# Kernel tuning notes

Measured on AMD Instinct MI355X. Metric: run time of the kernel, lower is better.

The kernel has to match this reference:

```python
import jax, jax.numpy as jnp
import numpy as np

TTT_STEPS = 1
STABILITY_LAMBDA = 0.01
TTT_LR = 0.01

def setup_inputs() -> dict:
    key = jax.random.key(0)
    ks = jax.random.split(key, 4)
    B, T, H = 8, 4096, 1024
    D = H // 4
    scale1 = 1.0 / np.sqrt(H)
    scale2 = 1.0 / np.sqrt(D)
    return {
        "state": jax.random.normal(ks[0], (B, T, H), dtype=jnp.float32),
        "target": jax.random.normal(ks[1], (B, T, H), dtype=jnp.float32),
        "W1": jax.random.normal(ks[2], (H, D), dtype=jnp.float32) * scale1,
        "b1": jnp.zeros((D,), dtype=jnp.float32),
        "W2": jax.random.normal(ks[3], (D, H), dtype=jnp.float32) * scale2,
        "b2": jnp.zeros((H,), dtype=jnp.float32),
        "step_size": jnp.float32(TTT_LR),
    }

def reference(state, target, W1, b1, W2, b2, step_size):
    # TTT: one (or more) gradient-descent steps on the state, minimizing
    # per-token MSE of a 2-layer MLP reconstruction + stability penalty.
    orig_state = state  # detached anchor

    def loss_fn(s):
        h = jax.nn.relu(jnp.einsum("bth,hd->btd", s, W1) + b1)
        pred = jnp.einsum("btd,dh->bth", h, W2) + b2
        # F.mse_loss(..., 'none').mean(-1) then .mean() == global mean of sq err
        mse = jnp.mean((pred - target) ** 2)
        stab = STABILITY_LAMBDA * jnp.mean((s - orig_state) ** 2)
        return mse + stab

    for _ in range(TTT_STEPS):
        g = jax.grad(loss_fn)(state)
        state = state - step_size * g
    return state
```

## Files before the change

### kernel.cpp

```cpp
#include <hip/hip_runtime.h>
#include <hip/hip_bf16.h>


#define Hdim 1024
#define Ddim 256
#define NTOK 32768
#define MT   32

typedef __attribute__((ext_vector_type(8))) short bf16x8;
typedef __attribute__((ext_vector_type(4))) float f32x4;

static __device__ __forceinline__ unsigned short f2bf(float f) {
    unsigned u = __builtin_bit_cast(unsigned, f);
    u += 0x7FFFu + ((u >> 16) & 1u);
    return (unsigned short)(u >> 16);
}

__global__ void prep_weights(const float* __restrict__ W1, const float* __restrict__ W2,
                             unsigned short* __restrict__ w1, unsigned short* __restrict__ w1t,
                             unsigned short* __restrict__ w2, unsigned short* __restrict__ w2t) {
    int i = blockIdx.x * blockDim.x + threadIdx.x;
    if (i >= Hdim * Ddim) return;
    int h = i / Ddim, d = i - h * Ddim;
    unsigned short v1 = f2bf(W1[i]);
    w1[i] = v1;
    w1t[d * Hdim + h] = v1;
    unsigned short v2 = f2bf(W2[d * Hdim + h]);
    w2[d * Hdim + h] = v2;
    w2t[i] = v2;
}

__launch_bounds__(256, 2)
__global__ void ttt_fused(const float* __restrict__ state,
                          const float* __restrict__ target,
                          const float* __restrict__ b1,
                          const float* __restrict__ b2,
                          const float* __restrict__ step_size,
                          const unsigned short* __restrict__ w1,
                          const unsigned short* __restrict__ w1t,
                          const unsigned short* __restrict__ w2,
                          const unsigned short* __restrict__ w2t,
                          float* __restrict__ out) {
    __shared__ unsigned char eld[MT * Hdim * 2];
    __shared__ unsigned char hld[MT * Ddim * 2];

    const int tid  = threadIdx.x;
    const int lane = tid & 63;
    const int wv   = tid >> 6;
    const int lr16 = lane & 15;
    const int lhi  = lane >> 4;
    const int kof  = lhi * 8;
    const int m0   = blockIdx.x * MT;

    const f32x4 z4 = {0.f, 0.f, 0.f, 0.f};

    {
        f32x4 acc[2][4];
        #pragma unroll
        for (int mt = 0; mt < 2; ++mt)
            #pragma unroll
            for (int nt = 0; nt < 4; ++nt) acc[mt][nt] = z4;

        for (int kk = 0; kk < Hdim; kk += 32) {
            bf16x8 a[2];
            #pragma unroll
            for (int mt = 0; mt < 2; ++mt) {
                const float* sr = state + (size_t)(m0 + mt * 16 + lr16) * Hdim + kk + kof;
                float4 f0 = *(const float4*)sr;
                float4 f1 = *(const float4*)(sr + 4);
                bf16x8 av;
                av[0] = (short)f2bf(f0.x); av[1] = (short)f2bf(f0.y);
                av[2] = (short)f2bf(f0.z); av[3] = (short)f2bf(f0.w);
                av[4] = (short)f2bf(f1.x); av[5] = (short)f2bf(f1.y);
                av[6] = (short)f2bf(f1.z); av[7] = (short)f2bf(f1.w);
                a[mt] = av;
            }
            #pragma unroll
            for (int nt = 0; nt < 4; ++nt) {
                int col = wv * 64 + nt * 16 + lr16;
                bf16x8 b = *(const bf16x8*)(w1t + (size_t)col * Hdim + kk + kof);
                #pragma unroll
                for (int mt = 0; mt < 2; ++mt)
                    acc[mt][nt] = __builtin_amdgcn_mfma_f32_16x16x32_bf16(a[mt], b, acc[mt][nt], 0, 0, 0);
            }
        }
        float bias[4];
        #pragma unroll
        for (int nt = 0; nt < 4; ++nt) bias[nt] = b1[wv * 64 + nt * 16 + lr16];
        #pragma unroll
        for (int mt = 0; mt < 2; ++mt)
            #pragma unroll
            for (int nt = 0; nt < 4; ++nt) {
                int colg = wv * 64 + nt * 16 + lr16;
                #pragma unroll
                for (int i = 0; i < 4; ++i) {
                    int row = mt * 16 + lhi * 4 + i;
                    float hv = fmaxf(acc[mt][nt][i] + bias[nt], 0.f);
                    unsigned off = ((unsigned)(row * Ddim + colg) * 2u) ^ (unsigned)((row & 7) << 4);
                    *(unsigned short*)(hld + off) = f2bf(hv);
                }
            }
    }
    __syncthreads();

    {
        for (int nc = 0; nc < 4; ++nc) {
            const int cb = wv * 256 + nc * 64;
            f32x4 acc[2][4];
            #pragma unroll
            for (int mt = 0; mt < 2; ++mt)
                #pragma unroll
                for (int nt = 0; nt < 4; ++nt) acc[mt][nt] = z4;

            for (int kk = 0; kk < Ddim; kk += 32) {
                bf16x8 a[2];
                #pragma unroll
                for (int mt = 0; mt < 2; ++mt) {
                    int row = mt * 16 + lr16;
                    unsigned off = ((unsigned)(row * Ddim + kk + kof) * 2u) ^ (unsigned)((row & 7) << 4);
                    a[mt] = *(const bf16x8*)(hld + off);
                }
                #pragma unroll
                for (int nt = 0; nt < 4; ++nt) {
                    int col = cb + nt * 16 + lr16;
                    bf16x8 b = *(const bf16x8*)(w2t + (size_t)col * Ddim + kk + kof);
                    #pragma unroll
                    for (int mt = 0; mt < 2; ++mt)
                        acc[mt][nt] = __builtin_amdgcn_mfma_f32_16x16x32_bf16(a[mt], b, acc[mt][nt], 0, 0, 0);
                }
            }
            float bias[4];
            #pragma unroll
            for (int nt = 0; nt < 4; ++nt) bias[nt] = b2[cb + nt * 16 + lr16];
            #pragma unroll
            for (int nt = 0; nt < 4; ++nt) {
                int colg = cb + nt * 16 + lr16;
                #pragma unroll
                for (int mt = 0; mt < 2; ++mt)
                    #pragma unroll
                    for (int i = 0; i < 4; ++i) {
                        int row = mt * 16 + lhi * 4 + i;
                        float e = acc[mt][nt][i] + bias[nt]
                                - target[(size_t)(m0 + row) * Hdim + colg];
                        unsigned off = ((unsigned)(row * Hdim + colg) * 2u) ^ (unsigned)((row & 7) << 4);
                        *(unsigned short*)(eld + off) = f2bf(e);
                    }
            }
        }
    }
    __syncthreads();

    {
        f32x4 acc[2][4];
        #pragma unroll
        for (int mt = 0; mt < 2; ++mt)
            #pragma unroll
            for (int nt = 0; nt < 4; ++nt) acc[mt][nt] = z4;

        for (int kk = 0; kk < Hdim; kk += 32) {
            bf16x8 a[2];
            #pragma unroll
            for (int mt = 0; mt < 2; ++mt) {
                int row = mt * 16 + lr16;
                unsigned off = ((unsigned)(row * Hdim + kk + kof) * 2u) ^ (unsigned)((row & 7) << 4);
                a[mt] = *(const bf16x8*)(eld + off);
            }
            #pragma unroll
            for (int nt = 0; nt < 4; ++nt) {
                int col = wv * 64 + nt * 16 + lr16;
                bf16x8 b = *(const bf16x8*)(w2 + (size_t)col * Hdim + kk + kof);
                #pragma unroll
                for (int mt = 0; mt < 2; ++mt)
                    acc[mt][nt] = __builtin_amdgcn_mfma_f32_16x16x32_bf16(a[mt], b, acc[mt][nt], 0, 0, 0);
            }
        }
        #pragma unroll
        for (int mt = 0; mt < 2; ++mt)
            #pragma unroll
            for (int nt = 0; nt < 4; ++nt) {
                int colg = wv * 64 + nt * 16 + lr16;
                #pragma unroll
                for (int i = 0; i < 4; ++i) {
                    int row = mt * 16 + lhi * 4 + i;
                    unsigned off = ((unsigned)(row * Ddim + colg) * 2u) ^ (unsigned)((row & 7) << 4);
                    unsigned short hbits = *(const unsigned short*)(hld + off);
                    float dh = (hbits != 0) ? acc[mt][nt][i] : 0.f;
                    *(unsigned short*)(hld + off) = f2bf(dh);
                }
            }
    }
    __syncthreads();

    {
        const float cc = step_size[0] * (2.0f / (float)((long long)NTOK * Hdim));
        for (int nc = 0; nc < 4; ++nc) {
            const int cb = wv * 256 + nc * 64;
            f32x4 acc[2][4];
            #pragma unroll
            for (int mt = 0; mt < 2; ++mt)
                #pragma unroll
                for (int nt = 0; nt < 4; ++nt) acc[mt][nt] = z4;

            for (int kk = 0; kk < Ddim; kk += 32) {
                bf16x8 a[2];
                #pragma unroll
                for (int mt = 0; mt < 2; ++mt) {
                    int row = mt * 16 + lr16;
                    unsigned off = ((unsigned)(row * Ddim + kk + kof) * 2u) ^ (unsigned)((row & 7) << 4);
                    a[mt] = *(const bf16x8*)(hld + off);
                }
                #pragma unroll
                for (int nt = 0; nt < 4; ++nt) {
                    int col = cb + nt * 16 + lr16;
                    bf16x8 b = *(const bf16x8*)(w1 + (size_t)col * Ddim + kk + kof);
                    #pragma unroll
                    for (int mt = 0; mt < 2; ++mt)
                        acc[mt][nt] = __builtin_amdgcn_mfma_f32_16x16x32_bf16(a[mt], b, acc[mt][nt], 0, 0, 0);
                }
            }
            #pragma unroll
            for (int nt = 0; nt < 4; ++nt) {
                int colg = cb + nt * 16 + lr16;
                #pragma unroll
                for (int mt = 0; mt < 2; ++mt)
                    #pragma unroll
                    for (int i = 0; i < 4; ++i) {
                        int row = mt * 16 + lhi * 4 + i;
                        size_t gi = (size_t)(m0 + row) * Hdim + colg;
                        out[gi] = state[gi] - cc * acc[mt][nt][i];
                    }
            }
        }
    }
}

extern "C" void kernel_launch(void* const* d_in, const int* in_sizes, int n_in,
                              void* d_out, int out_size, void* d_ws, size_t ws_size,
                              hipStream_t stream) {
    const float* state     = (const float*)d_in[0];
    const float* target    = (const float*)d_in[1];
    const float* W1        = (const float*)d_in[2];
    const float* b1        = (const float*)d_in[3];
    const float* W2        = (const float*)d_in[4];
    const float* b2        = (const float*)d_in[5];
    const float* step_size = (const float*)d_in[6];
    float* out = (float*)d_out;

    unsigned short* w1  = (unsigned short*)d_ws;
    unsigned short* w1t = w1  + Hdim * Ddim;
    unsigned short* w2  = w1t + Hdim * Ddim;
    unsigned short* w2t = w2  + Hdim * Ddim;

    hipLaunchKernelGGL(prep_weights, dim3((Hdim * Ddim + 255) / 256), dim3(256), 0, stream,
                       W1, W2, w1, w1t, w2, w2t);
    hipLaunchKernelGGL(ttt_fused, dim3(NTOK / MT), dim3(256), 0, stream,
                       state, target, b1, b2, step_size, w1, w1t, w2, w2t, out);
}
```

Measured before the change: 656.2 us.

## Precompute W2·W2ᵀ Gram matrix to skip output-space GEMMs in backward pass

Rewrites the error backprop as h·G + c2 − target·W2ᵀ using a precomputed Gram matrix G = W2·W2ᵀ and c2 = W2·b2. This removes the forward decoder GEMM and its backward counterpart over the 1024-wide hidden, and the large error buffer in shared memory. The target projection is fused into the first K-loop alongside the encoder GEMM. Blocks now use 512 threads split into two row groups. The cost is bf16 rounding of G and target, which changes numerics.

```diff
diff --git a/kernel.cpp b/kernel.cpp
--- a/kernel.cpp
+++ b/kernel.cpp
@@ -17,218 +17,179 @@
 }
 
 __global__ void prep_weights(const float* __restrict__ W1, const float* __restrict__ W2,
-                             unsigned short* __restrict__ w1, unsigned short* __restrict__ w1t,
-                             unsigned short* __restrict__ w2, unsigned short* __restrict__ w2t) {
+                             unsigned short* __restrict__ w1t,
+                             unsigned short* __restrict__ w2b,
+                             unsigned short* __restrict__ w1b) {
     int i = blockIdx.x * blockDim.x + threadIdx.x;
     if (i >= Hdim * Ddim) return;
-    int h = i / Ddim, d = i - h * Ddim;
+    int h = i >> 8, d = i & 255;
     unsigned short v1 = f2bf(W1[i]);
-    w1[i] = v1;
+    w1b[i] = v1;
     w1t[d * Hdim + h] = v1;
-    unsigned short v2 = f2bf(W2[d * Hdim + h]);
-    w2[d * Hdim + h] = v2;
-    w2t[i] = v2;
-}
-
-__launch_bounds__(256, 2)
+    w2b[i] = f2bf(W2[i]);
+}
+
+__global__ void prep_G(const float* __restrict__ W2, const float* __restrict__ b2,
+                       unsigned short* __restrict__ Gb, float* __restrict__ c2) {
+    __shared__ float wd[Hdim];
+    __shared__ float red[4];
+    const int d = blockIdx.x;
+    const int t = threadIdx.x;
+    float4 v = *(const float4*)(W2 + (size_t)d * Hdim + t * 4);
+    *(float4*)(wd + t * 4) = v;
+    __syncthreads();
+    const float* wp = W2 + (size_t)t * Hdim;
+    float s = 0.f;
+    for (int h = 0; h < Hdim; h += 4) {
+        float4 a = *(const float4*)(wp + h);
+        s += a.x * wd[h] + a.y * wd[h + 1] + a.z * wd[h + 2] + a.w * wd[h + 3];
+    }
+    Gb[d * Ddim + t] = f2bf(s);
+    float4 bb = *(const float4*)(b2 + t * 4);
+    float p = bb.x * wd[t * 4] + bb.y * wd[t * 4 + 1] + bb.z * wd[t * 4 + 2] + bb.w * wd[t * 4 + 3];
+    #pragma unroll
+    for (int o = 32; o > 0; o >>= 1) p += __shfl_down(p, o);
+    if ((t & 63) == 0) red[t >> 6] = p;
+    __syncthreads();
+    if (t == 0) c2[d] = red[0] + red[1] + red[2] + red[3];
+}
+
+__launch_bounds__(512, 4)
 __global__ void ttt_fused(const float* __restrict__ state,
                           const float* __restrict__ target,
                           const float* __restrict__ b1,
-                          const float* __restrict__ b2,
                           const float* __restrict__ step_size,
-                          const unsigned short* __restrict__ w1,
                           const unsigned short* __restrict__ w1t,
-                          const unsigned short* __restrict__ w2,
-                          const unsigned short* __restrict__ w2t,
+                          const unsigned short* __restrict__ w2b,
+                          const unsigned short* __restrict__ w1b,
+                          const unsigned short* __restrict__ Gb,
+                          const float* __restrict__ c2,
                           float* __restrict__ out) {
-    __shared__ unsigned char eld[MT * Hdim * 2];
     __shared__ unsigned char hld[MT * Ddim * 2];
+    __shared__ unsigned char dld[MT * Ddim * 2];
 
     const int tid  = threadIdx.x;
     const int lane = tid & 63;
     const int wv   = tid >> 6;
+    const int mg   = wv >> 2;
+    const int w4   = wv & 3;
     const int lr16 = lane & 15;
     const int lhi  = lane >> 4;
     const int kof  = lhi * 8;
     const int m0   = blockIdx.x * MT;
+    const int rowA = mg * 16 + lr16;
 
     const f32x4 z4 = {0.f, 0.f, 0.f, 0.f};
 
-    {
-        f32x4 acc[2][4];
-        #pragma unroll
-        for (int mt = 0; mt < 2; ++mt)
-            #pragma unroll
-            for (int nt = 0; nt < 4; ++nt) acc[mt][nt] = z4;
-
-        for (int kk = 0; kk < Hdim; kk += 32) {
-            bf16x8 a[2];
-            #pragma unroll
-            for (int mt = 0; mt < 2; ++mt) {
-                const float* sr = state + (size_t)(m0 + mt * 16 + lr16) * Hdim + kk + kof;
-                float4 f0 = *(const float4*)sr;
-                float4 f1 = *(const float4*)(sr + 4);
-                bf16x8 av;
-                av[0] = (short)f2bf(f0.x); av[1] = (short)f2bf(f0.y);
-                av[2] = (short)f2bf(f0.z); av[3] = (short)f2bf(f0.w);
-                av[4] = (short)f2bf(f1.x); av[5] = (short)f2bf(f1.y);
-                av[6] = (short)f2bf(f1.z); av[7] = (short)f2bf(f1.w);
-                a[mt] = av;
-            }
+    f32x4 acc_h[4], acc_u[4];
+    #pragma unroll
+    for (int nt = 0; nt < 4; ++nt) { acc_h[nt] = z4; acc_u[nt] = z4; }
+
+    const float* sp0 = state  + (size_t)(m0 + rowA) * Hdim + kof;
+    const float* tp0 = target + (size_t)(m0 + rowA) * Hdim + kof;
+
+    for (int kk = 0; kk < Hdim; kk += 32) {
+        float4 s0 = *(const float4*)(sp0 + kk);
+        float4 s1 = *(const float4*)(sp0 + kk + 4);
+        float4 t0 = *(const float4*)(tp0 + kk);
+        float4 t1 = *(const float4*)(tp0 + kk + 4);
+        bf16x8 aS, aT;
+        aS[0] = (short)f2bf(s0.x); aS[1] = (short)f2bf(s0.y);
+        aS[2] = (short)f2bf(s0.z); aS[3] = (short)f2bf(s0.w);
+        aS[4] = (short)f2bf(s1.x); aS[5] = (short)f2bf(s1.y);
+        aS[6] = (short)f2bf(s1.z); aS[7] = (short)f2bf(s1.w);
+        aT[0] = (short)f2bf(t0.x); aT[1] = (short)f2bf(t0.y);
+        aT[2] = (short)f2bf(t0.z); aT[3] = (short)f2bf(t0.w);
+        aT[4] = (short)f2bf(t1.x); aT[5] = (short)f2bf(t1.y);
+        aT[6] = (short)f2bf(t1.z); aT[7] = (short)f2bf(t1.w);
+        #pragma unroll
+        for (int nt = 0; nt < 4; ++nt) {
+            int col = w4 * 64 + nt * 16 + lr16;
+            bf16x8 bw1 = *(const bf16x8*)(w1t + (size_t)col * Hdim + kk + kof);
+            acc_h[nt] = __builtin_amdgcn_mfma_f32_16x16x32_bf16(aS, bw1, acc_h[nt], 0, 0, 0);
+            bf16x8 bw2 = *(const bf16x8*)(w2b + (size_t)col * Hdim + kk + kof);
+            acc_u[nt] = __builtin_amdgcn_mfma_f32_16x16x32_bf16(aT, bw2, acc_u[nt], 0, 0, 0);
+        }
+    }
+
+    unsigned mask = 0;
+    #pragma unroll
+    for (int nt = 0; nt < 4; ++nt) {
+        int colg = w4 * 64 + nt * 16 + lr16;
+        float bias = b1[colg];
+        #pragma unroll
+        for (int i = 0; i < 4; ++i) {
+            int row = mg * 16 + lhi * 4 + i;
+            float z = acc_h[nt][i] + bias;
+            if (z > 0.f) mask |= 1u << (nt * 4 + i);
+            float hv = z > 0.f ? z : 0.f;
+            unsigned off = ((unsigned)(row * Ddim + colg) * 2u) ^ (unsigned)((row & 7) << 4);
+            *(unsigned short*)(hld + off) = f2bf(hv);
+        }
+    }
+    __syncthreads();
+
+    f32x4 acc_d[4];
+    #pragma unroll
+    for (int nt = 0; nt < 4; ++nt) {
+        int colg = w4 * 64 + nt * 16 + lr16;
+        float c2v = c2[colg];
+        #pragma unroll
+        for (int i = 0; i < 4; ++i) acc_d[nt][i] = c2v - acc_u[nt][i];
+    }
+    #pragma unroll
+    for (int kk = 0; kk < Ddim; kk += 32) {
+        unsigned offa = ((unsigned)(rowA * Ddim + kk + kof) * 2u) ^ (unsigned)((rowA & 7) << 4);
+        bf16x8 aH = *(const bf16x8*)(hld + offa);
+        #pragma unroll
+        for (int nt = 0; nt < 4; ++nt) {
+            int col = w4 * 64 + nt * 16 + lr16;
+            bf16x8 bG = *(const bf16x8*)(Gb + (size_t)col * Ddim + kk + kof);
+            acc_d[nt] = __builtin_amdgcn_mfma_f32_16x16x32_bf16(aH, bG, acc_d[nt], 0, 0, 0);
+        }
+    }
+    #pragma unroll
+    for (int nt = 0; nt < 4; ++nt) {
+        int colg = w4 * 64 + nt * 16 + lr16;
+        #pragma unroll
+        for (int i = 0; i < 4; ++i) {
+            int row = mg * 16 + lhi * 4 + i;
+            float dh = ((mask >> (nt * 4 + i)) & 1u) ? acc_d[nt][i] : 0.f;
+            unsigned off = ((unsigned)(row * Ddim + colg) * 2u) ^ (unsigned)((row & 7) << 4);
+            *(unsigned short*)(dld + off) = f2bf(dh);
+        }
+    }
+    __syncthreads();
+
+    const float cc = step_size[0] * (2.0f / (float)((long long)NTOK * Hdim));
+    bf16x8 aD[8];
+    #pragma unroll
+    for (int kq = 0; kq < 8; ++kq) {
+        unsigned off = ((unsigned)(rowA * Ddim + kq * 32 + kof) * 2u) ^ (unsigned)((rowA & 7) << 4);
+        aD[kq] = *(const bf16x8*)(dld + off);
+    }
+    for (int nc = 0; nc < 4; ++nc) {
+        const int cb = w4 * 256 + nc * 64;
+        f32x4 acc[4];
+        #pragma unroll
+        for (int nt = 0; nt < 4; ++nt) acc[nt] = z4;
+        #pragma unroll
+        for (int kq = 0; kq < 8; ++kq) {
             #pragma unroll
             for (int nt = 0; nt < 4; ++nt) {
-                int col = wv * 64 + nt * 16 + lr16;
-                bf16x8 b = *(const bf16x8*)(w1t + (size_t)col * Hdim + kk + kof);
-                #pragma unroll
-                for (int mt = 0; mt < 2; ++mt)
-                    acc[mt][nt] = __builtin_amdgcn_mfma_f32_16x16x32_bf16(a[mt], b, acc[mt][nt], 0, 0, 0);
+                int col = cb + nt * 16 + lr16;
+                bf16x8 bW = *(const bf16x8*)(w1b + (size_t)col * Ddim + kq * 32 + kof);
+                acc[nt] = __builtin_amdgcn_mfma_f32_16x16x32_bf16(aD[kq], bW, acc[nt], 0, 0, 0);
             }
         }
-        float bias[4];
-        #pragma unroll
-        for (int nt = 0; nt < 4; ++nt) bias[nt] = b1[wv * 64 + nt * 16 + lr16];
-        #pragma unroll
-        for (int mt = 0; mt < 2; ++mt)
+        #pragma unroll
+        for (int nt = 0; nt < 4; ++nt) {
+            int colg = cb + nt * 16 + lr16;
             #pragma unroll
-            for (int nt = 0; nt < 4; ++nt) {
-                int colg = wv * 64 + nt * 16 + lr16;
-                #pragma unroll
-                for (int i = 0; i < 4; ++i) {
-                    int row = mt * 16 + lhi * 4 + i;
-                    float hv = fmaxf(acc[mt][nt][i] + bias[nt], 0.f);
-                    unsigned off = ((unsigned)(row * Ddim + colg) * 2u) ^ (unsigned)((row & 7) << 4);
-                    *(unsigned short*)(hld + off) = f2bf(hv);
-                }
-            }
-    }
-    __syncthreads();
-
-    {
-        for (int nc = 0; nc < 4; ++nc) {
-            const int cb = wv * 256 + nc * 64;
-            f32x4 acc[2][4];
-            #pragma unroll
-            for (int mt = 0; mt < 2; ++mt)
-                #pragma unroll
-                for (int nt = 0; nt < 4; ++nt) acc[mt][nt] = z4;
-
-            for (int kk = 0; kk < Ddim; kk += 32) {
-                bf16x8 a[2];
-                #pragma unroll
-                for (int mt = 0; mt < 2; ++mt) {
-                    int row = mt * 16 + lr16;
-                    unsigned off = ((unsigned)(row * Ddim + kk + kof) * 2u) ^ (unsigned)((row & 7) << 4);
-                    a[mt] = *(const bf16x8*)(hld + off);
-                }
-                #pragma unroll
-                for (int nt = 0; nt < 4; ++nt) {
-                    int col = cb + nt * 16 + lr16;
-                    bf16x8 b = *(const bf16x8*)(w2t + (size_t)col * Ddim + kk + kof);
-                    #pragma unroll
-                    for (int mt = 0; mt < 2; ++mt)
-                        acc[mt][nt] = __builtin_amdgcn_mfma_f32_16x16x32_bf16(a[mt], b, acc[mt][nt], 0, 0, 0);
-                }
-            }
-            float bias[4];
-            #pragma unroll
-            for (int nt = 0; nt < 4; ++nt) bias[nt] = b2[cb + nt * 16 + lr16];
-            #pragma unroll
-            for (int nt = 0; nt < 4; ++nt) {
-                int colg = cb + nt * 16 + lr16;
-                #pragma unroll
-                for (int mt = 0; mt < 2; ++mt)
-                    #pragma unroll
-                    for (int i = 0; i < 4; ++i) {
-                        int row = mt * 16 + lhi * 4 + i;
-                        float e = acc[mt][nt][i] + bias[nt]
-                                - target[(size_t)(m0 + row) * Hdim + colg];
-                        unsigned off = ((unsigned)(row * Hdim + colg) * 2u) ^ (unsigned)((row & 7) << 4);
-                        *(unsigned short*)(eld + off) = f2bf(e);
-                    }
-            }
-        }
-    }
-    __syncthreads();
-
-    {
-        f32x4 acc[2][4];
-        #pragma unroll
-        for (int mt = 0; mt < 2; ++mt)
-            #pragma unroll
-            for (int nt = 0; nt < 4; ++nt) acc[mt][nt] = z4;
-
-        for (int kk = 0; kk < Hdim; kk += 32) {
-            bf16x8 a[2];
-            #pragma unroll
-            for (int mt = 0; mt < 2; ++mt) {
-                int row = mt * 16 + lr16;
-                unsigned off = ((unsigned)(row * Hdim + kk + kof) * 2u) ^ (unsigned)((row & 7) << 4);
-                a[mt] = *(const bf16x8*)(eld + off);
-            }
-            #pragma unroll
-            for (int nt = 0; nt < 4; ++nt) {
-                int col = wv * 64 + nt * 16 + lr16;
-                bf16x8 b = *(const bf16x8*)(w2 + (size_t)col * Hdim + kk + kof);
-                #pragma unroll
-                for (int mt = 0; mt < 2; ++mt)
-                    acc[mt][nt] = __builtin_amdgcn_mfma_f32_16x16x32_bf16(a[mt], b, acc[mt][nt], 0, 0, 0);
-            }
-        }
-        #pragma unroll
-        for (int mt = 0; mt < 2; ++mt)
-            #pragma unroll
-            for (int nt = 0; nt < 4; ++nt) {
-                int colg = wv * 64 + nt * 16 + lr16;
-                #pragma unroll
-                for (int i = 0; i < 4; ++i) {
-                    int row = mt * 16 + lhi * 4 + i;
-                    unsigned off = ((unsigned)(row * Ddim + colg) * 2u) ^ (unsigned)((row & 7) << 4);
-                    unsigned short hbits = *(const unsigned short*)(hld + off);
-                    float dh = (hbits != 0) ? acc[mt][nt][i] : 0.f;
-                    *(unsigned short*)(hld + off) = f2bf(dh);
-                }
-            }
-    }
-    __syncthreads();
-
-    {
-        const float cc = step_size[0] * (2.0f / (float)((long long)NTOK * Hdim));
-        for (int nc = 0; nc < 4; ++nc) {
-            const int cb = wv * 256 + nc * 64;
-            f32x4 acc[2][4];
-            #pragma unroll
-            for (int mt = 0; mt < 2; ++mt)
-                #pragma unroll
-                for (int nt = 0; nt < 4; ++nt) acc[mt][nt] = z4;
-
-            for (int kk = 0; kk < Ddim; kk += 32) {
-                bf16x8 a[2];
-                #pragma unroll
-                for (int mt = 0; mt < 2; ++mt) {
-                    int row = mt * 16 + lr16;
-                    unsigned off = ((unsigned)(row * Ddim + kk + kof) * 2u) ^ (unsigned)((row & 7) << 4);
-                    a[mt] = *(const bf16x8*)(hld + off);
-                }
-                #pragma unroll
-                for (int nt = 0; nt < 4; ++nt) {
-                    int col = cb + nt * 16 + lr16;
-                    bf16x8 b = *(const bf16x8*)(w1 + (size_t)col * Ddim + kk + kof);
-                    #pragma unroll
-                    for (int mt = 0; mt < 2; ++mt)
-                        acc[mt][nt] = __builtin_amdgcn_mfma_f32_16x16x32_bf16(a[mt], b, acc[mt][nt], 0, 0, 0);
-                }
-            }
-            #pragma unroll
-            for (int nt = 0; nt < 4; ++nt) {
-                int colg = cb + nt * 16 + lr16;
-                #pragma unroll
-                for (int mt = 0; mt < 2; ++mt)
-                    #pragma unroll
-                    for (int i = 0; i < 4; ++i) {
-                        int row = mt * 16 + lhi * 4 + i;
-                        size_t gi = (size_t)(m0 + row) * Hdim + colg;
-                        out[gi] = state[gi] - cc * acc[mt][nt][i];
-                    }
+            for (int i = 0; i < 4; ++i) {
+                int row = mg * 16 + lhi * 4 + i;
+                size_t gi = (size_t)(m0 + row) * Hdim + colg;
+                out[gi] = state[gi] - cc * acc[nt][i];
             }
         }
     }
@@ -246,13 +207,15 @@
     const float* step_size = (const float*)d_in[6];
     float* out = (float*)d_out;
 
-    unsigned short* w1  = (unsigned short*)d_ws;
-    unsigned short* w1t = w1  + Hdim * Ddim;
-    unsigned short* w2  = w1t + Hdim * Ddim;
-    unsigned short* w2t = w2  + Hdim * Ddim;
+    unsigned short* w1t = (unsigned short*)d_ws;
+    unsigned short* w2b = w1t + Hdim * Ddim;
+    unsigned short* w1b = w2b + Hdim * Ddim;
+    unsigned short* Gb  = w1b + Hdim * Ddim;
+    float*          c2  = (float*)(Gb + Ddim * Ddim);
 
     hipLaunchKernelGGL(prep_weights, dim3((Hdim * Ddim + 255) / 256), dim3(256), 0, stream,
-                       W1, W2, w1, w1t, w2, w2t);
-    hipLaunchKernelGGL(ttt_fused, dim3(NTOK / MT), dim3(256), 0, stream,
-                       state, target, b1, b2, step_size, w1, w1t, w2, w2t, out);
-}
+                       W1, W2, w1t, w2b, w1b);
+    hipLaunchKernelGGL(prep_G, dim3(Ddim), dim3(256), 0, stream, W2, b2, Gb, c2);
+    hipLaunchKernelGGL(ttt_fused, dim3(NTOK / MT), dim3(512), 0, stream,
+                       state, target, b1, step_size, w1t, w2b, w1b, Gb, c2, out);
+}
```

New measurement: 763.4 us. 16.3% more time.

## Fold W2 into Gram matrix and fuse state/target projections with LDS-staged tiles

Applied to the files above, without the earlier changes.

Rewrites the backward pass algebraically. W2·(W2ᵀh + b2 − target) becomes h·G + c2 − target·W2ᵀ, with G = W2W2ᵀ and c2 = W2·b2 precomputed, so the H-wide error tensor is never materialized. The state·W1 and target·W2ᵀ projections run in one K-loop over 128-token tiles with LDS double-buffered staging and 512 threads. This removes one large GEMM and the error round-trip through LDS. In exchange it adds prep kernels, uses more LDS per block, and rounds G to bf16, which shifts the numerical error.

```diff
diff --git a/kernel.cpp b/kernel.cpp
--- a/kernel.cpp
+++ b/kernel.cpp
@@ -5,10 +5,13 @@
 #define Hdim 1024
 #define Ddim 256
 #define NTOK 32768
-#define MT   32
+#define MT   128
+#define KC   64
 
 typedef __attribute__((ext_vector_type(8))) short bf16x8;
 typedef __attribute__((ext_vector_type(4))) float f32x4;
+typedef __attribute__((ext_vector_type(4))) unsigned int u32x4;
+typedef unsigned short ushort_t;
 
 static __device__ __forceinline__ unsigned short f2bf(float f) {
     unsigned u = __builtin_bit_cast(unsigned, f);
@@ -16,222 +19,320 @@
     return (unsigned short)(u >> 16);
 }
 
-__global__ void prep_weights(const float* __restrict__ W1, const float* __restrict__ W2,
-                             unsigned short* __restrict__ w1, unsigned short* __restrict__ w1t,
-                             unsigned short* __restrict__ w2, unsigned short* __restrict__ w2t) {
-    int i = blockIdx.x * blockDim.x + threadIdx.x;
+static __device__ __forceinline__ bf16x8 pack8(float4 a, float4 b) {
+    bf16x8 v;
+    v[0] = (short)f2bf(a.x); v[1] = (short)f2bf(a.y);
+    v[2] = (short)f2bf(a.z); v[3] = (short)f2bf(a.w);
+    v[4] = (short)f2bf(b.x); v[5] = (short)f2bf(b.y);
+    v[6] = (short)f2bf(b.z); v[7] = (short)f2bf(b.w);
+    return v;
+}
+
+static __device__ __forceinline__ unsigned swz(unsigned byte_off, int row) {
+    return byte_off ^ ((unsigned)(row & 7) << 4);
+}
+
+__global__ void prep_copy(const float* __restrict__ W1, const float* __restrict__ W2,
+                          ushort_t* __restrict__ w1b, ushort_t* __restrict__ w2b) {
+    int i = (blockIdx.x * 256 + threadIdx.x) * 8;
     if (i >= Hdim * Ddim) return;
-    int h = i / Ddim, d = i - h * Ddim;
-    unsigned short v1 = f2bf(W1[i]);
-    w1[i] = v1;
-    w1t[d * Hdim + h] = v1;
-    unsigned short v2 = f2bf(W2[d * Hdim + h]);
-    w2[d * Hdim + h] = v2;
-    w2t[i] = v2;
-}
-
-__launch_bounds__(256, 2)
+    float4 a0 = *(const float4*)(W1 + i), a1 = *(const float4*)(W1 + i + 4);
+    *(bf16x8*)(w1b + i) = pack8(a0, a1);
+    float4 c0 = *(const float4*)(W2 + i), c1 = *(const float4*)(W2 + i + 4);
+    *(bf16x8*)(w2b + i) = pack8(c0, c1);
+}
+
+__global__ void prep_t(const float* __restrict__ W1, ushort_t* __restrict__ w1t) {
+    __shared__ ushort_t tile[64][72];
+    const int h0 = blockIdx.x * 64, d0 = blockIdx.y * 64;
+    const int t = threadIdx.x;
+    const int r = t >> 2, c4 = (t & 3) * 16;
+    #pragma unroll
+    for (int j = 0; j < 4; ++j) {
+        float4 v = *(const float4*)(W1 + (size_t)(h0 + r) * Ddim + d0 + c4 + j * 4);
+        tile[r][c4 + j * 4 + 0] = f2bf(v.x);
+        tile[r][c4 + j * 4 + 1] = f2bf(v.y);
+        tile[r][c4 + j * 4 + 2] = f2bf(v.z);
+        tile[r][c4 + j * 4 + 3] = f2bf(v.w);
+    }
+    __syncthreads();
+    const int dr = t >> 2, hc = (t & 3) * 16;
+    bf16x8 o0, o1;
+    #pragma unroll
+    for (int j = 0; j < 8; ++j) o0[j] = (short)tile[hc + j][dr];
+    #pragma unroll
+    for (int j = 0; j < 8; ++j) o1[j] = (short)tile[hc + 8 + j][dr];
+    *(bf16x8*)(w1t + (size_t)(d0 + dr) * Hdim + h0 + hc)     = o0;
+    *(bf16x8*)(w1t + (size_t)(d0 + dr) * Hdim + h0 + hc + 8) = o1;
+}
+
+__launch_bounds__(512, 2)
+__global__ void prep_G(const ushort_t* __restrict__ w2b, const float* __restrict__ W2,
+                       const float* __restrict__ b2, ushort_t* __restrict__ Gb,
+                       float* __restrict__ c2) {
+    const int tid = threadIdx.x, lane = tid & 63, wv = tid >> 6;
+    const int lr16 = lane & 15, lhi = lane >> 4;
+    const int rbase = blockIdx.x * 128 + (wv >> 2) * 64;
+    const int ngb = (wv & 3) * 64;
+    const f32x4 z4 = {0.f, 0.f, 0.f, 0.f};
+    f32x4 acc[4][4];
+    #pragma unroll
+    for (int mt = 0; mt < 4; ++mt)
+        #pragma unroll
+        for (int nt = 0; nt < 4; ++nt) acc[mt][nt] = z4;
+    #pragma unroll 4
+    for (int kk = 0; kk < 32; ++kk) {
+        bf16x8 aA[4], bB[4];
+        #pragma unroll
+        for (int mt = 0; mt < 4; ++mt)
+            aA[mt] = *(const bf16x8*)(w2b + (size_t)(rbase + mt * 16 + lr16) * Hdim + kk * 32 + lhi * 8);
+        #pragma unroll
+        for (int nt = 0; nt < 4; ++nt)
+            bB[nt] = *(const bf16x8*)(w2b + (size_t)(ngb + nt * 16 + lr16) * Hdim + kk * 32 + lhi * 8);
+        #pragma unroll
+        for (int mt = 0; mt < 4; ++mt)
+            #pragma unroll
+            for (int nt = 0; nt < 4; ++nt)
+                acc[mt][nt] = __builtin_amdgcn_mfma_f32_16x16x32_bf16(aA[mt], bB[nt], acc[mt][nt], 0, 0, 0);
+    }
+    #pragma unroll
+    for (int mt = 0; mt < 4; ++mt)
+        #pragma unroll
+        for (int nt = 0; nt < 4; ++nt) {
+            int col = ngb + nt * 16 + lr16;
+            #pragma unroll
+            for (int i = 0; i < 4; ++i) {
+                int row = rbase + mt * 16 + lhi * 4 + i;
+                Gb[row * Ddim + col] = f2bf(acc[mt][nt][i]);
+            }
+        }
+    if (blockIdx.x == 0 && tid < 256) {
+        const float* wp = W2 + (size_t)tid * Hdim;
+        float s0 = 0.f, s1 = 0.f;
+        for (int h = 0; h < Hdim; h += 8) {
+            float4 a = *(const float4*)(wp + h), b = *(const float4*)(wp + h + 4);
+            float4 x = *(const float4*)(b2 + h), y = *(const float4*)(b2 + h + 4);
+            s0 += a.x * x.x + a.y * x.y + a.z * x.z + a.w * x.w;
+            s1 += b.x * y.x + b.y * y.y + b.z * y.z + b.w * y.w;
+        }
+        c2[tid] = s0 + s1;
+    }
+}
+
+__launch_bounds__(512, 2)
 __global__ void ttt_fused(const float* __restrict__ state,
                           const float* __restrict__ target,
-                          const float* __restrict__ b1,
-                          const float* __restrict__ b2,
+                          const float* __restrict__ b1g,
                           const float* __restrict__ step_size,
-                          const unsigned short* __restrict__ w1,
-                          const unsigned short* __restrict__ w1t,
-                          const unsigned short* __restrict__ w2,
-                          const unsigned short* __restrict__ w2t,
+                          const ushort_t* __restrict__ w1t,
+                          const ushort_t* __restrict__ w2b,
+                          const ushort_t* __restrict__ w1b,
+                          const ushort_t* __restrict__ Gb,
+                          const float* __restrict__ c2,
                           float* __restrict__ out) {
-    __shared__ unsigned char eld[MT * Hdim * 2];
-    __shared__ unsigned char hld[MT * Ddim * 2];
+    __shared__ __align__(16) char smem[131072];
+    char* const sS  = smem;
+    char* const sT  = smem + 16384;
+    char* const sW1 = smem + 32768;
+    char* const sW2 = smem + 65536;
+    char* const hls = smem;
+    char* const dls = smem + 65536;
 
     const int tid  = threadIdx.x;
     const int lane = tid & 63;
     const int wv   = tid >> 6;
+    const int mgb  = (wv >> 2) * 64;
+    const int ng   = wv & 3;
+    const int ngb  = ng * 64;
     const int lr16 = lane & 15;
     const int lhi  = lane >> 4;
-    const int kof  = lhi * 8;
     const int m0   = blockIdx.x * MT;
 
+    const int srow = tid >> 2;
+    const int sc4  = (tid & 3) * 16;
+    const int wrow = tid >> 1;
+    const int wce  = (tid & 1) * 32;
+    const float* const spS = state  + (size_t)(m0 + srow) * Hdim + sc4;
+    const float* const spT = target + (size_t)(m0 + srow) * Hdim + sc4;
+    const ushort_t* const wpA = w1t + (size_t)wrow * Hdim + wce;
+    const ushort_t* const wpB = w2b + (size_t)wrow * Hdim + wce;
+    const unsigned offS0 = swz((unsigned)(srow * 128 + sc4 * 2), srow);
+    const unsigned offS1 = swz((unsigned)(srow * 128 + sc4 * 2 + 16), srow);
+    unsigned offW[4];
+    #pragma unroll
+    for (int j = 0; j < 4; ++j) offW[j] = swz((unsigned)(wrow * 128 + wce * 2 + j * 16), wrow);
+
     const f32x4 z4 = {0.f, 0.f, 0.f, 0.f};
-
+    f32x4 acc_h[4][4], acc_u[4][4];
+    #pragma unroll
+    for (int mt = 0; mt < 4; ++mt)
+        #pragma unroll
+        for (int nt = 0; nt < 4; ++nt) { acc_h[mt][nt] = z4; acc_u[mt][nt] = z4; }
+
+    float4 ps[4], pt[4];
+
+#define ISSUE(kc) { \
+    _Pragma("unroll") for (int j = 0; j < 4; ++j) ps[j] = *(const float4*)(spS + (kc) * KC + j * 4); \
+    _Pragma("unroll") for (int j = 0; j < 4; ++j) pt[j] = *(const float4*)(spT + (kc) * KC + j * 4); }
+
+#define STAGE(kc) { \
+    u32x4 pw[8]; \
+    _Pragma("unroll") for (int j = 0; j < 4; ++j) pw[j]     = *(const u32x4*)(wpA + (kc) * KC + j * 8); \
+    _Pragma("unroll") for (int j = 0; j < 4; ++j) pw[4 + j] = *(const u32x4*)(wpB + (kc) * KC + j * 8); \
+    *(bf16x8*)(sS + offS0) = pack8(ps[0], ps[1]); \
+    *(bf16x8*)(sS + offS1) = pack8(ps[2], ps[3]); \
+    *(bf16x8*)(sT + offS0) = pack8(pt[0], pt[1]); \
+    *(bf16x8*)(sT + offS1) = pack8(pt[2], pt[3]); \
+    _Pragma("unroll") for (int j = 0; j < 4; ++j) *(u32x4*)(sW1 + offW[j]) = pw[j]; \
+    _Pragma("unroll") for (int j = 0; j < 4; ++j) *(u32x4*)(sW2 + offW[j]) = pw[4 + j]; }
+
+#define COMPUTE() { \
+    _Pragma("unroll") for (int kk = 0; kk < 2; ++kk) { \
+        bf16x8 aS[4], aT[4], b1v[4], b2v[4]; \
+        _Pragma("unroll") for (int mt = 0; mt < 4; ++mt) { \
+            int r = mgb + mt * 16 + lr16; \
+            unsigned off = swz((unsigned)(r * 128 + kk * 64 + lhi * 16), r); \
+            aS[mt] = *(const bf16x8*)(sS + off); \
+            aT[mt] = *(const bf16x8*)(sT + off); \
+        } \
+        _Pragma("unroll") for (int nt = 0; nt < 4; ++nt) { \
+            int c = ngb + nt * 16 + lr16; \
+            unsigned off = swz((unsigned)(c * 128 + kk * 64 + lhi * 16), c); \
+            b1v[nt] = *(const bf16x8*)(sW1 + off); \
+            b2v[nt] = *(const bf16x8*)(sW2 + off); \
+        } \
+        _Pragma("unroll") for (int mt = 0; mt < 4; ++mt) \
+            _Pragma("unroll") for (int nt = 0; nt < 4; ++nt) { \
+                acc_h[mt][nt] = __builtin_amdgcn_mfma_f32_16x16x32_bf16(aS[mt], b1v[nt], acc_h[mt][nt], 0, 0, 0); \
+                acc_u[mt][nt] = __builtin_amdgcn_mfma_f32_16x16x32_bf16(aT[mt], b2v[nt], acc_u[mt][nt], 0, 0, 0); \
+            } \
+    } }
+
+    ISSUE(0);
+    STAGE(0);
+    ISSUE(1);
+    __syncthreads();
+    for (int kc = 0; kc < Hdim / KC; ++kc) {
+        COMPUTE();
+        __syncthreads();
+        if (kc < Hdim / KC - 1) {
+            STAGE(kc + 1);
+            if (kc < Hdim / KC - 2) ISSUE(kc + 2);
+            __syncthreads();
+        }
+    }
+
+    unsigned long long mask = 0ULL;
     {
-        f32x4 acc[2][4];
-        #pragma unroll
-        for (int mt = 0; mt < 2; ++mt)
-            #pragma unroll
-            for (int nt = 0; nt < 4; ++nt) acc[mt][nt] = z4;
-
-        for (int kk = 0; kk < Hdim; kk += 32) {
-            bf16x8 a[2];
-            #pragma unroll
-            for (int mt = 0; mt < 2; ++mt) {
-                const float* sr = state + (size_t)(m0 + mt * 16 + lr16) * Hdim + kk + kof;
-                float4 f0 = *(const float4*)sr;
-                float4 f1 = *(const float4*)(sr + 4);
-                bf16x8 av;
-                av[0] = (short)f2bf(f0.x); av[1] = (short)f2bf(f0.y);
-                av[2] = (short)f2bf(f0.z); av[3] = (short)f2bf(f0.w);
-                av[4] = (short)f2bf(f1.x); av[5] = (short)f2bf(f1.y);
-                av[6] = (short)f2bf(f1.z); av[7] = (short)f2bf(f1.w);
-                a[mt] = av;
-            }
+        float bia[4];
+        #pragma unroll
+        for (int nt = 0; nt < 4; ++nt) bia[nt] = b1g[ngb + nt * 16 + lr16];
+        #pragma unroll
+        for (int mt = 0; mt < 4; ++mt)
             #pragma unroll
             for (int nt = 0; nt < 4; ++nt) {
-                int col = wv * 64 + nt * 16 + lr16;
-                bf16x8 b = *(const bf16x8*)(w1t + (size_t)col * Hdim + kk + kof);
-                #pragma unroll
-                for (int mt = 0; mt < 2; ++mt)
-                    acc[mt][nt] = __builtin_amdgcn_mfma_f32_16x16x32_bf16(a[mt], b, acc[mt][nt], 0, 0, 0);
-            }
-        }
-        float bias[4];
-        #pragma unroll
-        for (int nt = 0; nt < 4; ++nt) bias[nt] = b1[wv * 64 + nt * 16 + lr16];
-        #pragma unroll
-        for (int mt = 0; mt < 2; ++mt)
+                int col = ngb + nt * 16 + lr16;
+                #pragma unroll
+                for (int i = 0; i < 4; ++i) {
+                    int row = mgb + mt * 16 + lhi * 4 + i;
+                    float z = acc_h[mt][nt][i] + bia[nt];
+                    float hv = z > 0.f ? z : 0.f;
+                    if (z > 0.f) mask |= 1ULL << (mt * 16 + nt * 4 + i);
+                    *(ushort_t*)(hls + swz((unsigned)(row * 512 + col * 2), row)) = f2bf(hv);
+                }
+            }
+    }
+    __syncthreads();
+
+    {
+        f32x4 acc_d[4][4];
+        #pragma unroll
+        for (int nt = 0; nt < 4; ++nt) {
+            float cv = c2[ngb + nt * 16 + lr16];
+            #pragma unroll
+            for (int mt = 0; mt < 4; ++mt)
+                #pragma unroll
+                for (int i = 0; i < 4; ++i) acc_d[mt][nt][i] = cv - acc_u[mt][nt][i];
+        }
+        #pragma unroll
+        for (int kk = 0; kk < 8; ++kk) {
+            bf16x8 aH[4], bG[4];
+            #pragma unroll
+            for (int mt = 0; mt < 4; ++mt) {
+                int r = mgb + mt * 16 + lr16;
+                aH[mt] = *(const bf16x8*)(hls + swz((unsigned)(r * 512 + kk * 64 + lhi * 16), r));
+            }
             #pragma unroll
             for (int nt = 0; nt < 4; ++nt) {
-                int colg = wv * 64 + nt * 16 + lr16;
+                int c = ngb + nt * 16 + lr16;
+                bG[nt] = *(const bf16x8*)(Gb + (size_t)c * Ddim + kk * 32 + lhi * 8);
+            }
+            #pragma unroll
+            for (int mt = 0; mt < 4; ++mt)
+                #pragma unroll
+                for (int nt = 0; nt < 4; ++nt)
+                    acc_d[mt][nt] = __builtin_amdgcn_mfma_f32_16x16x32_bf16(aH[mt], bG[nt], acc_d[mt][nt], 0, 0, 0);
+        }
+        #pragma unroll
+        for (int mt = 0; mt < 4; ++mt)
+            #pragma unroll
+            for (int nt = 0; nt < 4; ++nt) {
+                int col = ngb + nt * 16 + lr16;
                 #pragma unroll
                 for (int i = 0; i < 4; ++i) {
-                    int row = mt * 16 + lhi * 4 + i;
-                    float hv = fmaxf(acc[mt][nt][i] + bias[nt], 0.f);
-                    unsigned off = ((unsigned)(row * Ddim + colg) * 2u) ^ (unsigned)((row & 7) << 4);
-                    *(unsigned short*)(hld + off) = f2bf(hv);
+                    int row = mgb + mt * 16 + lhi * 4 + i;
+                    float v = ((mask >> (mt * 16 + nt * 4 + i)) & 1ULL) ? acc_d[mt][nt][i] : 0.f;
+                    *(ushort_t*)(dls + swz((unsigned)(row * 512 + col * 2), row)) = f2bf(v);
                 }
             }
     }
     __syncthreads();
 
     {
+        const float cc = step_size[0] * (2.0f / ((float)NTOK * (float)Hdim));
         for (int nc = 0; nc < 4; ++nc) {
-            const int cb = wv * 256 + nc * 64;
-            f32x4 acc[2][4];
-            #pragma unroll
-            for (int mt = 0; mt < 2; ++mt)
+            const int cb = ng * 256 + nc * 64;
+            f32x4 acc[4][4];
+            #pragma unroll
+            for (int mt = 0; mt < 4; ++mt)
                 #pragma unroll
                 for (int nt = 0; nt < 4; ++nt) acc[mt][nt] = z4;
-
-            for (int kk = 0; kk < Ddim; kk += 32) {
-                bf16x8 a[2];
-                #pragma unroll
-                for (int mt = 0; mt < 2; ++mt) {
-                    int row = mt * 16 + lr16;
-                    unsigned off = ((unsigned)(row * Ddim + kk + kof) * 2u) ^ (unsigned)((row & 7) << 4);
-                    a[mt] = *(const bf16x8*)(hld + off);
+            #pragma unroll
+            for (int kq = 0; kq < 8; ++kq) {
+                bf16x8 aD[4], bW[4];
+                #pragma unroll
+                for (int mt = 0; mt < 4; ++mt) {
+                    int r = mgb + mt * 16 + lr16;
+                    aD[mt] = *(const bf16x8*)(dls + swz((unsigned)(r * 512 + kq * 64 + lhi * 16), r));
                 }
                 #pragma unroll
                 for (int nt = 0; nt < 4; ++nt) {
-                    int col = cb + nt * 16 + lr16;
-                    bf16x8 b = *(const bf16x8*)(w2t + (size_t)col * Ddim + kk + kof);
+                    int c = cb + nt * 16 + lr16;
+                    bW[nt] = *(const bf16x8*)(w1b + (size_t)c * Ddim + kq * 32 + lhi * 8);
+                }
+                #pragma unroll
+                for (int mt = 0; mt < 4; ++mt)
                     #pragma unroll
-                    for (int mt = 0; mt < 2; ++mt)
-                        acc[mt][nt] = __builtin_amdgcn_mfma_f32_16x16x32_bf16(a[mt], b, acc[mt][nt], 0, 0, 0);
-                }
-            }
-            float bias[4];
-            #pragma unroll
-            for (int nt = 0; nt < 4; ++nt) bias[nt] = b2[cb + nt * 16 + lr16];
+                    for (int nt = 0; nt < 4; ++nt)
+                        acc[mt][nt] = __builtin_amdgcn_mfma_f32_16x16x32_bf16(aD[mt], bW[nt], acc[mt][nt], 0, 0, 0);
+            }
             #pragma unroll
             for (int nt = 0; nt < 4; ++nt) {
-                int colg = cb + nt * 16 + lr16;
-                #pragma unroll
-                for (int mt = 0; mt < 2; ++mt)
+                int col = cb + nt * 16 + lr16;
+                #pragma unroll
+                for (int mt = 0; mt < 4; ++mt)
                     #pragma unroll
                     for (int i = 0; i < 4; ++i) {
-                        int row = mt * 16 + lhi * 4 + i;
-                        float e = acc[mt][nt][i] + bias[nt]
-                                - target[(size_t)(m0 + row) * Hdim + colg];
-                        unsigned off = ((unsigned)(row * Hdim + colg) * 2u) ^ (unsigned)((row & 7) << 4);
-                        *(unsigned short*)(eld + off) = f2bf(e);
-                    }
-            }
-        }
-    }
-    __syncthreads();
-
-    {
-        f32x4 acc[2][4];
-        #pragma unroll
-        for (int mt = 0; mt < 2; ++mt)
-            #pragma unroll
-            for (int nt = 0; nt < 4; ++nt) acc[mt][nt] = z4;
-
-        for (int kk = 0; kk < Hdim; kk += 32) {
-            bf16x8 a[2];
-            #pragma unroll
-            for (int mt = 0; mt < 2; ++mt) {
-                int row = mt * 16 + lr16;
-                unsigned off = ((unsigned)(row * Hdim + kk + kof) * 2u) ^ (unsigned)((row & 7) << 4);
-                a[mt] = *(const bf16x8*)(eld + off);
-            }
-            #pragma unroll
-            for (int nt = 0; nt < 4; ++nt) {
-                int col = wv * 64 + nt * 16 + lr16;
-                bf16x8 b = *(const bf16x8*)(w2 + (size_t)col * Hdim + kk + kof);
-                #pragma unroll
-                for (int mt = 0; mt < 2; ++mt)
-                    acc[mt][nt] = __builtin_amdgcn_mfma_f32_16x16x32_bf16(a[mt], b, acc[mt][nt], 0, 0, 0);
-            }
-        }
-        #pragma unroll
-        for (int mt = 0; mt < 2; ++mt)
-            #pragma unroll
-            for (int nt = 0; nt < 4; ++nt) {
-                int colg = wv * 64 + nt * 16 + lr16;
-                #pragma unroll
-                for (int i = 0; i < 4; ++i) {
-                    int row = mt * 16 + lhi * 4 + i;
-                    unsigned off = ((unsigned)(row * Ddim + colg) * 2u) ^ (unsigned)((row & 7) << 4);
-                    unsigned short hbits = *(const unsigned short*)(hld + off);
-                    float dh = (hbits != 0) ? acc[mt][nt][i] : 0.f;
-                    *(unsigned short*)(hld + off) = f2bf(dh);
-                }
-            }
-    }
-    __syncthreads();
-
-    {
-        const float cc = step_size[0] * (2.0f / (float)((long long)NTOK * Hdim));
-        for (int nc = 0; nc < 4; ++nc) {
-            const int cb = wv * 256 + nc * 64;
-            f32x4 acc[2][4];
-            #pragma unroll
-            for (int mt = 0; mt < 2; ++mt)
-                #pragma unroll
-                for (int nt = 0; nt < 4; ++nt) acc[mt][nt] = z4;
-
-            for (int kk = 0; kk < Ddim; kk += 32) {
-                bf16x8 a[2];
-                #pragma unroll
-                for (int mt = 0; mt < 2; ++mt) {
-                    int row = mt * 16 + lr16;
-                    unsigned off = ((unsigned)(row * Ddim + kk + kof) * 2u) ^ (unsigned)((row & 7) << 4);
-                    a[mt] = *(const bf16x8*)(hld + off);
-                }
-                #pragma unroll
-                for (int nt = 0; nt < 4; ++nt) {
-                    int col = cb + nt * 16 + lr16;
-                    bf16x8 b = *(const bf16x8*)(w1 + (size_t)col * Ddim + kk + kof);
-                    #pragma unroll
-                    for (int mt = 0; mt < 2; ++mt)
-                        acc[mt][nt] = __builtin_amdgcn_mfma_f32_16x16x32_bf16(a[mt], b, acc[mt][nt], 0, 0, 0);
-                }
-            }
-            #pragma unroll
-            for (int nt = 0; nt < 4; ++nt) {
-                int colg = cb + nt * 16 + lr16;
-                #pragma unroll
-                for (int mt = 0; mt < 2; ++mt)
-                    #pragma unroll
-                    for (int i = 0; i < 4; ++i) {
-                        int row = mt * 16 + lhi * 4 + i;
-                        size_t gi = (size_t)(m0 + row) * Hdim + colg;
+                        int row = mgb + mt * 16 + lhi * 4 + i;
+                        size_t gi = (size_t)(m0 + row) * Hdim + col;
                         out[gi] = state[gi] - cc * acc[mt][nt][i];
                     }
             }
         }
     }
+#undef ISSUE
+#undef STAGE
+#undef COMPUTE
 }
 
 extern "C" void kernel_launch(void* const* d_in, const int* in_sizes, int n_in,
@@ -246,13 +347,15 @@
     const float* step_size = (const float*)d_in[6];
     float* out = (float*)d_out;
 
-    unsigned short* w1  = (unsigned short*)d_ws;
-    unsigned short* w1t = w1  + Hdim * Ddim;
-    unsigned short* w2  = w1t + Hdim * Ddim;
-    unsigned short* w2t = w2  + Hdim * Ddim;
-
-    hipLaunchKernelGGL(prep_weights, dim3((Hdim * Ddim + 255) / 256), dim3(256), 0, stream,
-                       W1, W2, w1, w1t, w2, w2t);
-    hipLaunchKernelGGL(ttt_fused, dim3(NTOK / MT), dim3(256), 0, stream,
-                       state, target, b1, b2, step_size, w1, w1t, w2, w2t, out);
-}
+    ushort_t* w1t = (ushort_t*)d_ws;
+    ushort_t* w1b = w1t + Hdim * Ddim;
+    ushort_t* w2b = w1b + Hdim * Ddim;
+    ushort_t* Gb  = w2b + Hdim * Ddim;
+    float*    c2  = (float*)(Gb + Ddim * Ddim);
+
+    hipLaunchKernelGGL(prep_copy, dim3(Hdim * Ddim / 8 / 256), dim3(256), 0, stream, W1, W2, w1b, w2b);
+    hipLaunchKernelGGL(prep_t, dim3(Hdim / 64, Ddim / 64), dim3(256), 0, stream, W1, w1t);
+    hipLaunchKernelGGL(prep_G, dim3(2), dim3(512), 0, stream, w2b, W2, b2, Gb, c2);
+    hipLaunchKernelGGL(ttt_fused, dim3(NTOK / MT), dim3(512), 0, stream,
+                       state, target, b1, step_size, w1t, w2b, w1b, Gb, c2, out);
+}
```

After: 581.5 us. 1.13x faster.
